# Kernel optimization log

Hardware: AMD Instinct MI355X
Metric: run time of the kernel (lower is better)

Reference implementation:

```python
import jax, jax.numpy as jnp
import numpy as np

GAMMA = 2.0
CONTINUITY_WEIGHT = 0.05
NUM_CLASSES = 3

B, L, C = 512, 16384, NUM_CLASSES


def setup_inputs() -> dict:
    key = jax.random.key(0)
    k1, k2, k3, k4, k5 = jax.random.split(key, 5)
    logits = jax.random.normal(k1, (B, L, C), dtype=jnp.float32)
    targets = jax.random.randint(k2, (B, L), 0, NUM_CLASSES, dtype=jnp.int32)
    mask = jnp.ones((B, L), dtype=jnp.bool_)
    # torchcrf initializes transitions Uniform(-0.1, 0.1); scaled normals are fine
    start_trans = jax.random.normal(k3, (C,), dtype=jnp.float32) * 0.1
    end_trans = jax.random.normal(k4, (C,), dtype=jnp.float32) * 0.1
    trans = jax.random.normal(k5, (C, C), dtype=jnp.float32) * 0.1
    return {"logits": logits, "targets": targets, "mask": mask,
            "start_trans": start_trans, "end_trans": end_trans, "trans": trans}


def _crf_neg_log_likelihood(emissions, tags, maskf, start_trans, end_trans, trans):
    # emissions: [B,L,C] fp32, tags: [B,L] int, maskf: [B,L] fp32 (mask[:,0]==1)
    Bb = emissions.shape[0]
    batch_idx = jnp.arange(Bb)
    # t = 0
    score0 = start_trans[tags[:, 0]] + emissions[batch_idx, 0, tags[:, 0]]  # [B]
    alpha0 = start_trans[None, :] + emissions[:, 0]                          # [B,C]

    # time-major slices for t = 1..L-1
    em_s = jnp.swapaxes(emissions[:, 1:], 0, 1)      # [L-1,B,C]
    tag_s = jnp.swapaxes(tags[:, 1:], 0, 1)          # [L-1,B]
    tagp_s = jnp.swapaxes(tags[:, :-1], 0, 1)        # [L-1,B]
    m_s = jnp.swapaxes(maskf[:, 1:], 0, 1)           # [L-1,B]

    def step(carry, xs):
        alpha, score = carry
        em_t, tag_t, tag_prev, m_t = xs
        # numerator: gold-path score
        s = trans[tag_prev, tag_t] + em_t[batch_idx, tag_t]
        score = score + s * m_t
        # denominator: forward algorithm
        nxt = jax.nn.logsumexp(alpha[:, :, None] + trans[None, :, :] + em_t[:, None, :], axis=1)
        alpha = jnp.where(m_t[:, None] > 0, nxt, alpha)
        return (alpha, score), None

    (alpha, score), _ = jax.lax.scan(step, (alpha0, score0), (em_s, tag_s, tagp_s, m_s))

    seq_ends = jnp.sum(maskf, axis=1).astype(jnp.int32) - 1
    last_tags = tags[batch_idx, seq_ends]
    numerator = score + end_trans[last_tags]                      # [B]
    denominator = jax.nn.logsumexp(alpha + end_trans[None, :], axis=1)  # [B]
    llh = numerator - denominator
    return -jnp.mean(llh)  # torchcrf reduction='mean' is mean over batch


def reference(logits, targets, mask, start_trans, end_trans, trans):
    Cc = logits.shape[-1]
    mask_b = mask.astype(jnp.bool_)
    valid = mask_b & (targets >= 0) & (targets < Cc)
    validf = valid.astype(jnp.float32)

    # focal loss over valid tokens
    tgt_safe = jnp.clip(targets, 0, Cc - 1)
    logp = jax.nn.log_softmax(logits, axis=-1)
    ce = -jnp.take_along_axis(logp, tgt_safe[..., None], axis=-1)[..., 0]  # [B,L]
    pt = jnp.exp(-ce)
    focal_tok = (1.0 - pt) ** GAMMA * ce
    n_valid = jnp.maximum(jnp.sum(validf), 1.0)
    focal = jnp.sum(focal_tok * validf) / n_valid

    # CRF loss (ignore_index remapped to 0, masked out in the score anyway when mask=0)
    tags_crf = jnp.where(targets < 0, 0, tgt_safe)
    maskf = mask_b.astype(jnp.float32)
    crf_loss = _crf_neg_log_likelihood(logits.astype(jnp.float32), tags_crf, maskf,
                                       start_trans, end_trans, trans)

    # continuity loss on predicted label transitions
    pred = jnp.argmax(logits, axis=-1)
    transitions = (pred[:, 1:] != pred[:, :-1]).astype(jnp.float32)
    v1 = validf[:, 1:]
    n_trans = jnp.maximum(jnp.sum(v1), 1.0)
    continuity = jnp.sum(transitions * v1) / n_trans

    total = focal + crf_loss + CONTINUITY_WEIGHT * continuity
    return total
```

## Files before the change

### kernel.cpp

```cpp
#include <hip/hip_runtime.h>
#include <hip/hip_bf16.h>

#define B_DIM 512
#define L_DIM 16384
#define TPB   512
#define KSTEPS 32
#define NGROUP 4
#define CONT_W  0.05f

#define LOG2E 1.4426950408889634f
#define LN2F  0.6931471805599453f

#if __has_builtin(__builtin_amdgcn_exp2f)
#define EXP2F(x) __builtin_amdgcn_exp2f(x)
#else
#define EXP2F(x) exp2f(x)
#endif
#if __has_builtin(__builtin_amdgcn_logf)
#define LOG2F(x) __builtin_amdgcn_logf(x)
#else
#define LOG2F(x) log2f(x)
#endif
#if __has_builtin(__builtin_amdgcn_rcpf)
#define RCPF(x) __builtin_amdgcn_rcpf(x)
#else
#define RCPF(x) (1.0f / (x))
#endif

__device__ __forceinline__ float lse2_3(float a, float b, float c) {
    float m = fmaxf(fmaxf(a, b), c);
    float s = EXP2F(a - m) + EXP2F(b - m) + EXP2F(c - m);
    return m + LOG2F(s);
}

__device__ __forceinline__ float sel3(int k, float a, float b, float c) {
    return (k == 0) ? a : ((k == 1) ? b : c);
}

__global__ __launch_bounds__(TPB) void pass1(
    const float* __restrict__ logits,
    const int* __restrict__ targets,
    const int* __restrict__ mask,
    const float* __restrict__ trans,
    float* __restrict__ partials)
{
    const int b   = blockIdx.x;
    const int tid = threadIdx.x;
    const size_t base = (size_t)b * L_DIM;

    const float t00 = trans[0]*LOG2E, t01 = trans[1]*LOG2E, t02 = trans[2]*LOG2E;
    const float t10 = trans[3]*LOG2E, t11 = trans[4]*LOG2E, t12 = trans[5]*LOG2E;
    const float t20 = trans[6]*LOG2E, t21 = trans[7]*LOG2E, t22 = trans[8]*LOG2E;
    const float w00 = EXP2F(t00), w01 = EXP2F(t01), w02 = EXP2F(t02);
    const float w10 = EXP2F(t10), w11 = EXP2F(t11), w12 = EXP2F(t12);
    const float w20 = EXP2F(t20), w21 = EXP2F(t21), w22 = EXP2F(t22);

    const int t0 = tid * KSTEPS;

    float p00 = 1.f, p01 = 0.f, p02 = 0.f;
    float p10 = 0.f, p11 = 1.f, p12 = 0.f;
    float p20 = 0.f, p21 = 0.f, p22 = 1.f;
    float s_acc = 0.f;

    int pred_prev = 0, tag_prev = 0;
    if (t0 > 0) {
        const float* r = logits + (base + t0 - 1) * 3;
        float a = r[0], bb = r[1], c = r[2];
        pred_prev = (bb > a) ? ((c > bb) ? 2 : 1) : ((c > a) ? 2 : 0);
        int tp = targets[base + t0 - 1];
        tag_prev = (tp < 0) ? 0 : ((tp > 2) ? 2 : tp);
    }

    float score2 = 0.f, focalP = 0.f, nvalidP = 0.f;
    float ntransP = 0.f, tcountP = 0.f, mcountP = 0.f;

    auto doStep = [&](int t, float e0, float e1, float e2, int tgt, int mkv) {
        const bool mb = (mkv != 0);
        mcountP += mb ? 1.f : 0.f;
        const bool valid = mb && (tgt >= 0) && (tgt < 3);
        const int  tag   = (tgt < 0) ? 0 : ((tgt > 2) ? 2 : tgt);
        const float f0 = e0 * LOG2E, f1 = e1 * LOG2E, f2 = e2 * LOG2E;
        const float E0 = EXP2F(f0), E1 = EXP2F(f1), E2 = EXP2F(f2);
        const float S  = E0 + E1 + E2;
        const float ftag = sel3(tag, f0, f1, f2);
        const float ce2 = LOG2F(S) - ftag;
        const float pt  = sel3(tag, E0, E1, E2) * RCPF(S);
        const float om  = 1.f - pt;
        if (valid) { focalP += om * om * (ce2 * LN2F); nvalidP += 1.f; }
        const int pred = (e1 > e0) ? ((e2 > e1) ? 2 : 1) : ((e2 > e0) ? 2 : 0);
        if (t >= 1) {
            if (valid) { ntransP += 1.f; tcountP += (pred != pred_prev) ? 1.f : 0.f; }
            if (mb) {
                const float c0 = sel3(tag, t00, t01, t02);
                const float c1 = sel3(tag, t10, t11, t12);
                const float c2 = sel3(tag, t20, t21, t22);
                score2 += sel3(tag_prev, c0, c1, c2) + ftag;
                const float a00 = w00*E0, a01 = w01*E1, a02 = w02*E2;
                const float a10 = w10*E0, a11 = w11*E1, a12 = w12*E2;
                const float a20 = w20*E0, a21 = w21*E1, a22 = w22*E2;
                const float n00 = p00*a00 + p01*a10 + p02*a20;
                const float n01 = p00*a01 + p01*a11 + p02*a21;
                const float n02 = p00*a02 + p01*a12 + p02*a22;
                const float n10 = p10*a00 + p11*a10 + p12*a20;
                const float n11 = p10*a01 + p11*a11 + p12*a21;
                const float n12 = p10*a02 + p11*a12 + p12*a22;
                const float n20 = p20*a00 + p21*a10 + p22*a20;
                const float n21 = p20*a01 + p21*a11 + p22*a21;
                const float n22 = p20*a02 + p21*a12 + p22*a22;
                p00 = n00; p01 = n01; p02 = n02;
                p10 = n10; p11 = n11; p12 = n12;
                p20 = n20; p21 = n21; p22 = n22;
            }
        }
        pred_prev = pred; tag_prev = tag;
    };

    const float4* Lp = reinterpret_cast<const float4*>(logits + (base + (size_t)t0) * 3);
    const int4*   Tp = reinterpret_cast<const int4*>(targets + base + t0);
    const int4*   Mp = reinterpret_cast<const int4*>(mask    + base + t0);

    #pragma unroll 1
    for (int g = 0; g < NGROUP; ++g) {
        float la[24]; int ta[8]; int ma[8];
        #pragma unroll
        for (int j = 0; j < 6; ++j)
            *reinterpret_cast<float4*>(&la[4 * j]) = Lp[g * 6 + j];
        *reinterpret_cast<int4*>(&ta[0]) = Tp[g * 2 + 0];
        *reinterpret_cast<int4*>(&ta[4]) = Tp[g * 2 + 1];
        *reinterpret_cast<int4*>(&ma[0]) = Mp[g * 2 + 0];
        *reinterpret_cast<int4*>(&ma[4]) = Mp[g * 2 + 1];

        const int tg = t0 + g * 8;
        #pragma unroll
        for (int u = 0; u < 8; ++u)
            doStep(tg + u, la[u * 3 + 0], la[u * 3 + 1], la[u * 3 + 2], ta[u], ma[u]);

        float mx = fmaxf(fmaxf(fmaxf(fmaxf(p00, p01), fmaxf(p02, p10)),
                               fmaxf(fmaxf(p11, p12), fmaxf(p20, p21))), p22);
        const unsigned bbits = __float_as_uint(mx);
        const int ex = (int)((bbits >> 23) & 255u) - 127;
        const float sc = __uint_as_float((unsigned)(127 - ex) << 23);
        p00 *= sc; p01 *= sc; p02 *= sc;
        p10 *= sc; p11 *= sc; p12 *= sc;
        p20 *= sc; p21 *= sc; p22 *= sc;
        s_acc += (float)ex;
    }

    __shared__ float sP[TPB][10];
    __shared__ float sS[TPB][6];
    sP[tid][0] = p00; sP[tid][1] = p01; sP[tid][2] = p02;
    sP[tid][3] = p10; sP[tid][4] = p11; sP[tid][5] = p12;
    sP[tid][6] = p20; sP[tid][7] = p21; sP[tid][8] = p22;
    sP[tid][9] = s_acc;
    sS[tid][0] = score2; sS[tid][1] = focalP; sS[tid][2] = nvalidP;
    sS[tid][3] = ntransP; sS[tid][4] = tcountP; sS[tid][5] = mcountP;
    __syncthreads();

    for (int off = 1; off < TPB; off <<= 1) {
        if ((tid & (2 * off - 1)) == 0) {
            float A[9], Bm[9], Cn[9];
            #pragma unroll
            for (int k = 0; k < 9; ++k) { A[k] = sP[tid][k]; Bm[k] = sP[tid + off][k]; }
            float s = sP[tid][9] + sP[tid + off][9];
            #pragma unroll
            for (int i = 0; i < 3; ++i)
                #pragma unroll
                for (int j = 0; j < 3; ++j)
                    Cn[i * 3 + j] = A[i * 3 + 0] * Bm[0 * 3 + j]
                                  + A[i * 3 + 1] * Bm[1 * 3 + j]
                                  + A[i * 3 + 2] * Bm[2 * 3 + j];
            float mx = Cn[0];
            #pragma unroll
            for (int k = 1; k < 9; ++k) mx = fmaxf(mx, Cn[k]);
            const unsigned bbits = __float_as_uint(mx);
            const int ex = (int)((bbits >> 23) & 255u) - 127;
            const float sc = __uint_as_float((unsigned)(127 - ex) << 23);
            #pragma unroll
            for (int k = 0; k < 9; ++k) sP[tid][k] = Cn[k] * sc;
            sP[tid][9] = s + (float)ex;
            #pragma unroll
            for (int k = 0; k < 6; ++k) sS[tid][k] += sS[tid + off][k];
        }
        __syncthreads();
    }

    if (tid == 0) {
        float* o = partials + (size_t)b * 16;
        #pragma unroll
        for (int k = 0; k < 10; ++k) o[k] = sP[0][k];
        #pragma unroll
        for (int k = 0; k < 6; ++k) o[10 + k] = sS[0][k];
    }
}

__global__ __launch_bounds__(B_DIM) void pass2(
    const float* __restrict__ logits,
    const int* __restrict__ targets,
    const float* __restrict__ start_trans,
    const float* __restrict__ end_trans,
    const float* __restrict__ partials,
    float* __restrict__ out)
{
    const int tid = threadIdx.x;
    double v_llh, v_focal, v_nv, v_nt, v_tc;

    {
        const int b = tid;
        const float* pp = partials + (size_t)b * 16;
        float P[9];
        #pragma unroll
        for (int k = 0; k < 9; ++k) P[k] = pp[k];
        const float s_scale = pp[9];
        const float score2  = pp[10];
        v_focal = (double)pp[11];
        v_nv    = (double)pp[12];
        v_nt    = (double)pp[13];
        v_tc    = (double)pp[14];
        const float mcount = pp[15];

        const size_t base = (size_t)b * L_DIM;
        const float e0 = logits[base * 3 + 0];
        const float e1 = logits[base * 3 + 1];
        const float e2 = logits[base * 3 + 2];
        const int tg0  = targets[base];
        const int tag0 = (tg0 < 0) ? 0 : ((tg0 > 2) ? 2 : tg0);

        const float a0 = (start_trans[0] + e0) * LOG2E;
        const float a1 = (start_trans[1] + e1) * LOG2E;
        const float a2 = (start_trans[2] + e2) * LOG2E;
        const float am = fmaxf(fmaxf(a0, a1), a2);
        const float al0 = EXP2F(a0 - am), al1 = EXP2F(a1 - am), al2 = EXP2F(a2 - am);
        const float af0 = al0 * P[0] + al1 * P[3] + al2 * P[6];
        const float af1 = al0 * P[1] + al1 * P[4] + al2 * P[7];
        const float af2 = al0 * P[2] + al1 * P[5] + al2 * P[8];
        const float et0 = EXP2F(end_trans[0] * LOG2E);
        const float et1 = EXP2F(end_trans[1] * LOG2E);
        const float et2 = EXP2F(end_trans[2] * LOG2E);
        const float d   = af0 * et0 + af1 * et1 + af2 * et2;
        const float den = (LOG2F(d) + am + s_scale) * LN2F;

        int seq_end = (int)(mcount + 0.5f) - 1;
        if (seq_end < 0) seq_end = 0;
        const int ltg = targets[base + seq_end];
        const int last_tag = (ltg < 0) ? 0 : ((ltg > 2) ? 2 : ltg);

        const float sc0 = start_trans[tag0] + sel3(tag0, e0, e1, e2);
        const float numer = sc0 + score2 * LN2F + end_trans[last_tag];
        v_llh = (double)numer - (double)den;
    }

    __shared__ double sred[B_DIM];
    double tot[5];
    double vals[5] = { v_llh, v_focal, v_nv, v_nt, v_tc };
    for (int q = 0; q < 5; ++q) {
        sred[tid] = vals[q];
        __syncthreads();
        for (int off = B_DIM / 2; off > 0; off >>= 1) {
            if (tid < off) sred[tid] += sred[tid + off];
            __syncthreads();
        }
        if (tid == 0) tot[q] = sred[0];
        __syncthreads();
    }

    if (tid == 0) {
        double nvv = (tot[2] > 1.0) ? tot[2] : 1.0;
        double ntt = (tot[3] > 1.0) ? tot[3] : 1.0;
        double focal_mean = tot[1] / nvv;
        double crf = -(tot[0] / (double)B_DIM);
        double cont = tot[4] / ntt;
        out[0] = (float)(focal_mean + crf + (double)CONT_W * cont);
    }
}

extern "C" void kernel_launch(void* const* d_in, const int* in_sizes, int n_in,
                              void* d_out, int out_size, void* d_ws, size_t ws_size,
                              hipStream_t stream) {
    const float* logits       = (const float*)d_in[0];
    const int*   targets      = (const int*)d_in[1];
    const int*   mask         = (const int*)d_in[2];
    const float* start_trans  = (const float*)d_in[3];
    const float* end_trans    = (const float*)d_in[4];
    const float* trans        = (const float*)d_in[5];
    float* out = (float*)d_out;
    float* partials = (float*)d_ws;

    pass1<<<B_DIM, TPB, 0, stream>>>(logits, targets, mask, trans, partials);
    pass2<<<1, B_DIM, 0, stream>>>(logits, targets, start_trans, end_trans, partials, out);
}
```

Before: 251.5 us.

## Split each sequence across four blocks and combine transfer matrices in finalize

Each sequence is now handled by four 256-thread blocks, each covering a quarter of the sequence with 16 steps per thread. Each block writes its partial 3x3 transfer matrix and scale, and finalize multiplies the four together. The scalar sums are accumulated with global float atomics into a memset workspace instead of being reduced in the final kernel. This raises the block count to spread work over more CUs and shortens the per-block scan chain. In exchange it adds a memset launch, atomic contention, and nondeterministic float summation order.

```diff
diff --git a/kernel.cpp b/kernel.cpp
--- a/kernel.cpp
+++ b/kernel.cpp
@@ -3,13 +3,18 @@
 
 #define B_DIM 512
 #define L_DIM 16384
-#define TPB   512
-#define KSTEPS 32
-#define NGROUP 4
+#define BLK_PER_SEQ 4
+#define SEG_LEN (L_DIM / BLK_PER_SEQ)
+#define TPB   256
+#define KSTEPS 16
+#define NGROUP 2
 #define CONT_W  0.05f
 
 #define LOG2E 1.4426950408889634f
 #define LN2F  0.6931471805599453f
+
+#define WS_ACC  20480
+#define WS_MC   20488
 
 #if __has_builtin(__builtin_amdgcn_exp2f)
 #define EXP2F(x) __builtin_amdgcn_exp2f(x)
@@ -27,12 +32,6 @@
 #define RCPF(x) (1.0f / (x))
 #endif
 
-__device__ __forceinline__ float lse2_3(float a, float b, float c) {
-    float m = fmaxf(fmaxf(a, b), c);
-    float s = EXP2F(a - m) + EXP2F(b - m) + EXP2F(c - m);
-    return m + LOG2F(s);
-}
-
 __device__ __forceinline__ float sel3(int k, float a, float b, float c) {
     return (k == 0) ? a : ((k == 1) ? b : c);
 }
@@ -42,11 +41,12 @@
     const int* __restrict__ targets,
     const int* __restrict__ mask,
     const float* __restrict__ trans,
-    float* __restrict__ partials)
+    float* __restrict__ ws)
 {
-    const int b   = blockIdx.x;
+    const int seq = blockIdx.x >> 2;
+    const int blk = blockIdx.x & 3;
     const int tid = threadIdx.x;
-    const size_t base = (size_t)b * L_DIM;
+    const size_t base = (size_t)seq * L_DIM;
 
     const float t00 = trans[0]*LOG2E, t01 = trans[1]*LOG2E, t02 = trans[2]*LOG2E;
     const float t10 = trans[3]*LOG2E, t11 = trans[4]*LOG2E, t12 = trans[5]*LOG2E;
@@ -55,7 +55,7 @@
     const float w10 = EXP2F(t10), w11 = EXP2F(t11), w12 = EXP2F(t12);
     const float w20 = EXP2F(t20), w21 = EXP2F(t21), w22 = EXP2F(t22);
 
-    const int t0 = tid * KSTEPS;
+    const int t0 = blk * SEG_LEN + tid * KSTEPS;
 
     float p00 = 1.f, p01 = 0.f, p02 = 0.f;
     float p10 = 0.f, p11 = 1.f, p12 = 0.f;
@@ -185,38 +185,50 @@
     }
 
     if (tid == 0) {
-        float* o = partials + (size_t)b * 16;
+        float* o = ws + (size_t)blockIdx.x * 10;
         #pragma unroll
         for (int k = 0; k < 10; ++k) o[k] = sP[0][k];
-        #pragma unroll
-        for (int k = 0; k < 6; ++k) o[10 + k] = sS[0][k];
+        atomicAdd(&ws[WS_ACC + 0], sS[0][0]);
+        atomicAdd(&ws[WS_ACC + 1], sS[0][1]);
+        atomicAdd(&ws[WS_ACC + 2], sS[0][2]);
+        atomicAdd(&ws[WS_ACC + 3], sS[0][3]);
+        atomicAdd(&ws[WS_ACC + 4], sS[0][4]);
+        atomicAdd(&ws[WS_MC + seq], sS[0][5]);
     }
 }
 
-__global__ __launch_bounds__(B_DIM) void pass2(
+__global__ __launch_bounds__(B_DIM) void finalize(
     const float* __restrict__ logits,
     const int* __restrict__ targets,
     const float* __restrict__ start_trans,
     const float* __restrict__ end_trans,
-    const float* __restrict__ partials,
+    const float* __restrict__ ws,
     float* __restrict__ out)
 {
-    const int tid = threadIdx.x;
-    double v_llh, v_focal, v_nv, v_nt, v_tc;
+    const int b = threadIdx.x;
+    double v_llh;
 
     {
-        const int b = tid;
-        const float* pp = partials + (size_t)b * 16;
-        float P[9];
-        #pragma unroll
-        for (int k = 0; k < 9; ++k) P[k] = pp[k];
-        const float s_scale = pp[9];
-        const float score2  = pp[10];
-        v_focal = (double)pp[11];
-        v_nv    = (double)pp[12];
-        v_nt    = (double)pp[13];
-        v_tc    = (double)pp[14];
-        const float mcount = pp[15];
+        const float* m0 = ws + (size_t)(b * 4 + 0) * 10;
+        float M[9];
+        #pragma unroll
+        for (int k = 0; k < 9; ++k) M[k] = m0[k];
+        float s_scale = m0[9];
+        #pragma unroll
+        for (int q = 1; q < 4; ++q) {
+            const float* mq = ws + (size_t)(b * 4 + q) * 10;
+            float N[9];
+            #pragma unroll
+            for (int i = 0; i < 3; ++i)
+                #pragma unroll
+                for (int j = 0; j < 3; ++j)
+                    N[i * 3 + j] = M[i * 3 + 0] * mq[0 * 3 + j]
+                                 + M[i * 3 + 1] * mq[1 * 3 + j]
+                                 + M[i * 3 + 2] * mq[2 * 3 + j];
+            #pragma unroll
+            for (int k = 0; k < 9; ++k) M[k] = N[k];
+            s_scale += mq[9];
+        }
 
         const size_t base = (size_t)b * L_DIM;
         const float e0 = logits[base * 3 + 0];
@@ -230,45 +242,45 @@
         const float a2 = (start_trans[2] + e2) * LOG2E;
         const float am = fmaxf(fmaxf(a0, a1), a2);
         const float al0 = EXP2F(a0 - am), al1 = EXP2F(a1 - am), al2 = EXP2F(a2 - am);
-        const float af0 = al0 * P[0] + al1 * P[3] + al2 * P[6];
-        const float af1 = al0 * P[1] + al1 * P[4] + al2 * P[7];
-        const float af2 = al0 * P[2] + al1 * P[5] + al2 * P[8];
+        const float af0 = al0 * M[0] + al1 * M[3] + al2 * M[6];
+        const float af1 = al0 * M[1] + al1 * M[4] + al2 * M[7];
+        const float af2 = al0 * M[2] + al1 * M[5] + al2 * M[8];
         const float et0 = EXP2F(end_trans[0] * LOG2E);
         const float et1 = EXP2F(end_trans[1] * LOG2E);
         const float et2 = EXP2F(end_trans[2] * LOG2E);
         const float d   = af0 * et0 + af1 * et1 + af2 * et2;
         const float den = (LOG2F(d) + am + s_scale) * LN2F;
 
+        const float mcount = ws[WS_MC + b];
         int seq_end = (int)(mcount + 0.5f) - 1;
         if (seq_end < 0) seq_end = 0;
         const int ltg = targets[base + seq_end];
         const int last_tag = (ltg < 0) ? 0 : ((ltg > 2) ? 2 : ltg);
 
         const float sc0 = start_trans[tag0] + sel3(tag0, e0, e1, e2);
-        const float numer = sc0 + score2 * LN2F + end_trans[last_tag];
-        v_llh = (double)numer - (double)den;
+        v_llh = (double)(sc0 + end_trans[last_tag]) - (double)den;
     }
 
     __shared__ double sred[B_DIM];
-    double tot[5];
-    double vals[5] = { v_llh, v_focal, v_nv, v_nt, v_tc };
-    for (int q = 0; q < 5; ++q) {
-        sred[tid] = vals[q];
+    sred[b] = v_llh;
+    __syncthreads();
+    for (int off = B_DIM / 2; off > 0; off >>= 1) {
+        if (b < off) sred[b] += sred[b + off];
         __syncthreads();
-        for (int off = B_DIM / 2; off > 0; off >>= 1) {
-            if (tid < off) sred[tid] += sred[tid + off];
-            __syncthreads();
-        }
-        if (tid == 0) tot[q] = sred[0];
-        __syncthreads();
-    }
-
-    if (tid == 0) {
-        double nvv = (tot[2] > 1.0) ? tot[2] : 1.0;
-        double ntt = (tot[3] > 1.0) ? tot[3] : 1.0;
-        double focal_mean = tot[1] / nvv;
-        double crf = -(tot[0] / (double)B_DIM);
-        double cont = tot[4] / ntt;
+    }
+
+    if (b == 0) {
+        const double score_sum = (double)ws[WS_ACC + 0] * (double)LN2F;
+        const double focal_sum = (double)ws[WS_ACC + 1];
+        const double nv        = (double)ws[WS_ACC + 2];
+        const double nt        = (double)ws[WS_ACC + 3];
+        const double tc        = (double)ws[WS_ACC + 4];
+        const double total_llh = sred[0] + score_sum;
+        const double nvv = (nv > 1.0) ? nv : 1.0;
+        const double ntt = (nt > 1.0) ? nt : 1.0;
+        const double focal_mean = focal_sum / nvv;
+        const double crf = -(total_llh / (double)B_DIM);
+        const double cont = tc / ntt;
         out[0] = (float)(focal_mean + crf + (double)CONT_W * cont);
     }
 }
@@ -283,8 +295,11 @@
     const float* end_trans    = (const float*)d_in[4];
     const float* trans        = (const float*)d_in[5];
     float* out = (float*)d_out;
-    float* partials = (float*)d_ws;
-
-    pass1<<<B_DIM, TPB, 0, stream>>>(logits, targets, mask, trans, partials);
-    pass2<<<1, B_DIM, 0, stream>>>(logits, targets, start_trans, end_trans, partials, out);
+    float* ws  = (float*)d_ws;
+
+    hipMemsetAsync((char*)d_ws + WS_ACC * sizeof(float), 0,
+                   (8 + B_DIM) * sizeof(float), stream);
+
+    pass1<<<B_DIM * BLK_PER_SEQ, TPB, 0, stream>>>(logits, targets, mask, trans, ws);
+    finalize<<<1, B_DIM, 0, stream>>>(logits, targets, start_trans, end_trans, ws, out);
 }
```

Result: slower. 310.6 us (+23.5%).
